# Optimization experiments

Measured on AMD Instinct MI355X. Metric: run time of the kernel, lower is better.

The kernel has to match this reference:

```python
import jax, jax.numpy as jnp
import numpy as np


def setup_inputs() -> dict:
    key = jax.random.key(0)
    ks = jax.random.split(key, 6)
    SEQ, B, N_INP, N_HID, N_OUT = 2048, 128, 64, 128, 10
    # orthogonal-ish init scales (rand_ortho produces orthogonal matrices; we use
    # scaled gaussians as stand-ins since exact values don't affect the op pattern)
    x = jax.random.normal(ks[0], (SEQ, B, N_INP), dtype=jnp.float32)
    Wxh = jax.random.normal(ks[1], (N_INP, N_HID), dtype=jnp.float32) * np.sqrt(1.0 / N_INP).astype(np.float32)
    Whh = jax.random.normal(ks[2], (N_HID, N_HID), dtype=jnp.float32) * np.sqrt(1.0 / N_HID).astype(np.float32)
    Why = jax.random.normal(ks[3], (N_HID, N_OUT), dtype=jnp.float32) * np.sqrt(1.0 / N_HID).astype(np.float32)
    bh = jnp.zeros((N_HID,), dtype=jnp.float32)
    by = jnp.zeros((N_OUT,), dtype=jnp.float32)
    return {"x": x, "Wxh": Wxh, "Whh": Whh, "Why": Why, "bh": bh, "by": by}


def reference(x, Wxh, Whh, Why, bh, by):
    # x: [seq_len, batch, n_inp]
    seq_len, batch, _ = x.shape
    n_hid = Whh.shape[0]
    # precompute the input projection for all timesteps in one big GEMM
    xW = jnp.einsum('sbi,ih->sbh', x, Wxh) + bh  # [S, B, H]

    def step(h_prev, xw_t):
        h_t = jnp.tanh(h_prev @ Whh + xw_t)
        return h_t, h_t

    h0 = jnp.zeros((batch, n_hid), dtype=x.dtype)
    h_last, h = jax.lax.scan(step, h0, xW)  # h: [S, B, H]
    logits = h_last @ Why + by  # [B, n_out]
    return (logits, h)
```

## Files before the change

### kernel.cpp

```cpp
#include <hip/hip_runtime.h>
#include <math.h>

#define SEQ   2048
#define BATCH  128
#define NINP    64
#define NHID   128
#define NOUT    10
#define CH      64
#define NCHUNK (SEQ / CH)

typedef const float __attribute__((address_space(1)))* gptr_t;
typedef float       __attribute__((address_space(3)))* lptr_t;

__global__ __launch_bounds__(256) void proj_kernel(const float* __restrict__ x,
                                                   const float* __restrict__ Wxh,
                                                   const float* __restrict__ bh,
                                                   float* __restrict__ xw) {
    __shared__ float Wlds[NINP * NHID];
    __shared__ float xs[32 * NINP];
    const int t = threadIdx.x;
    const size_t r0 = (size_t)blockIdx.x * 32;

#pragma unroll
    for (int i = 0; i < 8; ++i)
        ((float4*)Wlds)[t + 256 * i] = ((const float4*)Wxh)[t + 256 * i];
    const float4* xg = (const float4*)(x + r0 * NINP);
    ((float4*)xs)[t]       = xg[t];
    ((float4*)xs)[t + 256] = xg[t + 256];
    __syncthreads();

    const int tj = t & 31;
    const int tr = t >> 5;
    const int j  = 4 * tj;
    const float4 bhv = *(const float4*)(bh + j);
    float acc[4][4];
#pragma unroll
    for (int r = 0; r < 4; ++r) {
        acc[r][0] = bhv.x; acc[r][1] = bhv.y; acc[r][2] = bhv.z; acc[r][3] = bhv.w;
    }
#pragma unroll 8
    for (int i = 0; i < NINP; ++i) {
        const float4 w4 = *(const float4*)&Wlds[i * NHID + j];
#pragma unroll
        for (int r = 0; r < 4; ++r) {
            const float xv = xs[(4 * tr + r) * NINP + i];
            acc[r][0] = fmaf(xv, w4.x, acc[r][0]);
            acc[r][1] = fmaf(xv, w4.y, acc[r][1]);
            acc[r][2] = fmaf(xv, w4.z, acc[r][2]);
            acc[r][3] = fmaf(xv, w4.w, acc[r][3]);
        }
    }
#pragma unroll
    for (int r = 0; r < 4; ++r) {
        float4 o = { acc[r][0], acc[r][1], acc[r][2], acc[r][3] };
        *(float4*)(xw + (r0 + 4 * tr + r) * NHID + j) = o;
    }
}

__global__ __launch_bounds__(256) void scan_kernel(const float* __restrict__ Whh,
                                                   float* __restrict__ hbuf) {
    __shared__ float xwc[2][CH][NHID];
    __shared__ float hs[2][NHID];

    const int b = blockIdx.x;
    const int t = threadIdx.x;
    const int w = t >> 6;
    const int l = t & 63;
    const int j = 32 * w + (l & 31);
    const int half = l >> 5;
    const bool writer = (l < 32);

    float wreg[64];
    {
        const float* wp = Whh + (size_t)(64 * half) * NHID + j;
#pragma unroll
        for (int kk = 0; kk < 64; ++kk) wreg[kk] = wp[(size_t)kk * NHID];
#pragma unroll
        for (int kk = 0; kk < 64; ++kk) asm volatile("" : "+v"(wreg[kk]));
    }

    hs[0][t & 127] = 0.f;
    hs[1][t & 127] = 0.f;

    float* rowbase = hbuf + (size_t)b * NHID;

    auto issue_chunk = [&](int c, int nb) {
#pragma unroll
        for (int i = 0; i < 8; ++i) {
            const int f  = (i * 4 + w) * 256 + l * 4;
            const int tl = f >> 7;
            const int jj = f & 127;
            const float* gp = hbuf + ((size_t)(c * CH + tl) * BATCH + b) * NHID + jj;
            lptr_t lp = (lptr_t)&xwc[nb][0][0] + (i * 4 + w) * 256;
            __builtin_amdgcn_global_load_lds((gptr_t)gp, lp, 16, 0, 0);
        }
    };

    issue_chunk(0, 0);
    asm volatile("s_waitcnt vmcnt(0)" ::: "memory");
    __syncthreads();

    int cbuf = 0;
    for (int c = 0; c < NCHUNK; ++c) {
        if (c + 1 < NCHUNK) issue_chunk(c + 1, cbuf ^ 1);
        const float (*xwcur)[NHID] = xwc[cbuf];

        for (int ts = 0; ts < CH; ++ts) {
            const float* hp = &hs[ts & 1][64 * half];
            float a0 = 0.f, a1 = 0.f, a2 = 0.f, a3 = 0.f;
#pragma unroll
            for (int q = 0; q < 16; ++q) {
                const float4 h4 = *(const float4*)(hp + 4 * q);
                a0 = fmaf(h4.x, wreg[4 * q + 0], a0);
                a1 = fmaf(h4.y, wreg[4 * q + 1], a1);
                a2 = fmaf(h4.z, wreg[4 * q + 2], a2);
                a3 = fmaf(h4.w, wreg[4 * q + 3], a3);
            }
            float acc = (a0 + a1) + (a2 + a3);
            acc += __shfl_xor(acc, 32, 64);

            if (writer) {
                const float z  = acc + xwcur[ts][j];
                const float zc = fminf(fmaxf(z, -15.f), 15.f);
                const float e  = __builtin_amdgcn_exp2f(zc * 2.8853900817779268f);
                const float hv = (e - 1.f) * __builtin_amdgcn_rcpf(e + 1.f);
                hs[(ts & 1) ^ 1][j] = hv;
                rowbase[(size_t)(c * CH + ts) * BATCH * NHID + j] = hv;
            }
            asm volatile("s_waitcnt lgkmcnt(0)" ::: "memory");
            __builtin_amdgcn_s_barrier();
            __builtin_amdgcn_sched_barrier(0);
        }

        asm volatile("s_waitcnt vmcnt(0)" ::: "memory");
        __builtin_amdgcn_s_barrier();
        __builtin_amdgcn_sched_barrier(0);
        cbuf ^= 1;
    }
}

__global__ __launch_bounds__(256) void head_kernel(const float* __restrict__ hlast,
                                                   const float* __restrict__ Why,
                                                   const float* __restrict__ by,
                                                   float* __restrict__ out) {
    const int idx = blockIdx.x * 256 + threadIdx.x;
    if (idx >= BATCH * NOUT) return;
    const int b = idx / NOUT;
    const int o = idx % NOUT;
    const float* h = hlast + (size_t)b * NHID;
    float acc = by[o];
#pragma unroll 8
    for (int k = 0; k < NHID; ++k)
        acc = fmaf(h[k], Why[(size_t)k * NOUT + o], acc);
    out[idx] = acc;
}

extern "C" void kernel_launch(void* const* d_in, const int* in_sizes, int n_in,
                              void* d_out, int out_size, void* d_ws, size_t ws_size,
                              hipStream_t stream) {
    const float* x   = (const float*)d_in[0];
    const float* Wxh = (const float*)d_in[1];
    const float* Whh = (const float*)d_in[2];
    const float* Why = (const float*)d_in[3];
    const float* bh  = (const float*)d_in[4];
    const float* by  = (const float*)d_in[5];
    float* out  = (float*)d_out;
    float* hreg = out + BATCH * NOUT;

    proj_kernel<<<(SEQ * BATCH) / 32, 256, 0, stream>>>(x, Wxh, bh, hreg);
    scan_kernel<<<BATCH, 256, 0, stream>>>(Whh, hreg);
    head_kernel<<<5, 256, 0, stream>>>(hreg + (size_t)(SEQ - 1) * BATCH * NHID,
                                       Why, by, out);
}
```

Before: 1.230 ms.

## Split recurrent matvec by input rows across waves using readlane broadcast

Restructures the per-step h@Whh product so that each wave owns 32 input rows of Whh and broadcasts its own hidden values with readlane, rather than having every thread read the whole h vector from LDS. Each wave writes partial sums for all 128 outputs to LDS, and after one barrier every wave reduces the four partials for its 32 outputs and applies tanh. This removes the LDS reads of h and the cross-half shuffle, at the cost of more LDS partial-sum traffic and 32 scalar readlanes per step. The loop is also unrolled by two.

After: 1.220 ms. About the same (-0.8%).

```diff
diff --git a/kernel.cpp b/kernel.cpp
--- a/kernel.cpp
+++ b/kernel.cpp
@@ -60,27 +60,29 @@
 __global__ __launch_bounds__(256) void scan_kernel(const float* __restrict__ Whh,
                                                    float* __restrict__ hbuf) {
     __shared__ float xwc[2][CH][NHID];
-    __shared__ float hs[2][NHID];
+    __shared__ float P[2][4][NHID];
 
-    const int b = blockIdx.x;
-    const int t = threadIdx.x;
-    const int w = t >> 6;
-    const int l = t & 63;
-    const int j = 32 * w + (l & 31);
-    const int half = l >> 5;
-    const bool writer = (l < 32);
+    const int b  = blockIdx.x;
+    const int t  = threadIdx.x;
+    const int w  = t >> 6;
+    const int l  = t & 63;
+    const int jj = l & 31;
+    const int j0 = 32 * w;
 
-    float wreg[64];
+    float wx[32], wy[32];
     {
-        const float* wp = Whh + (size_t)(64 * half) * NHID + j;
+        const float* wp = Whh + (size_t)j0 * NHID + l;
 #pragma unroll
-        for (int kk = 0; kk < 64; ++kk) wreg[kk] = wp[(size_t)kk * NHID];
+        for (int i = 0; i < 32; ++i) {
+            wx[i] = wp[(size_t)i * NHID];
+            wy[i] = wp[(size_t)i * NHID + 64];
+        }
 #pragma unroll
-        for (int kk = 0; kk < 64; ++kk) asm volatile("" : "+v"(wreg[kk]));
+        for (int i = 0; i < 32; ++i) {
+            asm volatile("" : "+v"(wx[i]));
+            asm volatile("" : "+v"(wy[i]));
+        }
     }
-
-    hs[0][t & 127] = 0.f;
-    hs[1][t & 127] = 0.f;
 
     float* rowbase = hbuf + (size_t)b * NHID;
 
@@ -89,8 +91,8 @@
         for (int i = 0; i < 8; ++i) {
             const int f  = (i * 4 + w) * 256 + l * 4;
             const int tl = f >> 7;
-            const int jj = f & 127;
-            const float* gp = hbuf + ((size_t)(c * CH + tl) * BATCH + b) * NHID + jj;
+            const int jx = f & 127;
+            const float* gp = hbuf + ((size_t)(c * CH + tl) * BATCH + b) * NHID + jx;
             lptr_t lp = (lptr_t)&xwc[nb][0][0] + (i * 4 + w) * 256;
             __builtin_amdgcn_global_load_lds((gptr_t)gp, lp, 16, 0, 0);
         }
@@ -100,36 +102,45 @@
     asm volatile("s_waitcnt vmcnt(0)" ::: "memory");
     __syncthreads();
 
+    float vh = 0.f;
     int cbuf = 0;
+
     for (int c = 0; c < NCHUNK; ++c) {
         if (c + 1 < NCHUNK) issue_chunk(c + 1, cbuf ^ 1);
-        const float (*xwcur)[NHID] = xwc[cbuf];
 
+#pragma unroll 2
         for (int ts = 0; ts < CH; ++ts) {
-            const float* hp = &hs[ts & 1][64 * half];
-            float a0 = 0.f, a1 = 0.f, a2 = 0.f, a3 = 0.f;
+            const int pb = ts & 1;
+            const float xwv = xwc[cbuf][ts][j0 + jj];
+
+            float ax = 0.f, ay = 0.f;
 #pragma unroll
-            for (int q = 0; q < 16; ++q) {
-                const float4 h4 = *(const float4*)(hp + 4 * q);
-                a0 = fmaf(h4.x, wreg[4 * q + 0], a0);
-                a1 = fmaf(h4.y, wreg[4 * q + 1], a1);
-                a2 = fmaf(h4.z, wreg[4 * q + 2], a2);
-                a3 = fmaf(h4.w, wreg[4 * q + 3], a3);
+            for (int i = 0; i < 32; ++i) {
+                const float hr = __uint_as_float(
+                    __builtin_amdgcn_readlane(__float_as_uint(vh), i));
+                ax = fmaf(hr, wx[i], ax);
+                ay = fmaf(hr, wy[i], ay);
             }
-            float acc = (a0 + a1) + (a2 + a3);
-            acc += __shfl_xor(acc, 32, 64);
+            P[pb][w][l]      = ax;
+            P[pb][w][l + 64] = ay;
 
-            if (writer) {
-                const float z  = acc + xwcur[ts][j];
-                const float zc = fminf(fmaxf(z, -15.f), 15.f);
-                const float e  = __builtin_amdgcn_exp2f(zc * 2.8853900817779268f);
-                const float hv = (e - 1.f) * __builtin_amdgcn_rcpf(e + 1.f);
-                hs[(ts & 1) ^ 1][j] = hv;
-                rowbase[(size_t)(c * CH + ts) * BATCH * NHID + j] = hv;
-            }
             asm volatile("s_waitcnt lgkmcnt(0)" ::: "memory");
             __builtin_amdgcn_s_barrier();
             __builtin_amdgcn_sched_barrier(0);
+
+            const float p0 = P[pb][0][j0 + jj];
+            const float p1 = P[pb][1][j0 + jj];
+            const float p2 = P[pb][2][j0 + jj];
+            const float p3 = P[pb][3][j0 + jj];
+            const float z  = ((p0 + p1) + (p2 + p3)) + xwv;
+
+            const float zc = fminf(fmaxf(z, -15.f), 15.f);
+            const float e  = __builtin_amdgcn_exp2f(zc * 2.8853900817779268f);
+            const float hv = (e - 1.f) * __builtin_amdgcn_rcpf(e + 1.f);
+            vh = hv;
+
+            if (l < 32)
+                rowbase[(size_t)(c * CH + ts) * BATCH * NHID + j0 + l] = hv;
         }
 
         asm volatile("s_waitcnt vmcnt(0)" ::: "memory");
```
